# Kernel optimization log

Measured on AMD Instinct MI355X. Metric: run time of the kernel, lower is better.

The kernel has to match this reference:

```python
import jax, jax.numpy as jnp
import numpy as np

THETA = 10000.0
NUM_HEADS = 16


def _rope(x, token_positions):
    # x: [B, H, S, d_k], token_positions: [B, S]
    d_k = x.shape[-1]
    half = d_k // 2
    k = jnp.arange(half, dtype=jnp.float32)
    inv_k = THETA ** (-2.0 * k / d_k)                      # [half]
    pos = token_positions.astype(jnp.float32)              # [B, S]
    angles = pos[..., None] * inv_k                         # [B, S, half]
    angles = jnp.repeat(angles, 2, axis=-1)                 # [B, S, d_k] interleaved
    cos = jnp.cos(angles)[:, None]                          # [B, 1, S, d_k]
    sin = jnp.sin(angles)[:, None]
    x_even = x[..., ::2]
    x_odd = x[..., 1::2]
    r_x = jnp.stack((-x_odd, x_even), axis=-1).reshape(x.shape)
    return x * cos + r_x * sin


def setup_inputs() -> dict:
    key = jax.random.key(0)
    ks = jax.random.split(key, 6)
    B, S, D = 4, 2048, 1024
    delta = 2.0 / np.sqrt(D + D)
    x = jax.random.normal(ks[0], (B, S, D), dtype=jnp.float32)
    Wq = jax.random.normal(ks[1], (D, D), dtype=jnp.float32) * delta
    Wk = jax.random.normal(ks[2], (D, D), dtype=jnp.float32) * delta
    Wv = jax.random.normal(ks[3], (D, D), dtype=jnp.float32) * delta
    Wo = jax.random.normal(ks[4], (D, D), dtype=jnp.float32) * delta
    token_positions = jnp.broadcast_to(jnp.arange(S, dtype=jnp.int64), (B, S))
    return {"x": x, "Wq": Wq, "Wk": Wk, "Wv": Wv, "Wo": Wo,
            "token_positions": token_positions}


def reference(x, Wq, Wk, Wv, Wo, token_positions):
    B, S, D = x.shape
    H = NUM_HEADS
    d_k = D // H

    def split_heads(t):
        return t.reshape(B, S, H, d_k).transpose(0, 2, 1, 3)  # [B, H, S, d_k]

    q = split_heads(x @ Wq.T)
    k = split_heads(x @ Wk.T)
    v = split_heads(x @ Wv.T)

    q = _rope(q, token_positions)
    k = _rope(k, token_positions)

    scores = jnp.einsum('bhqd,bhkd->bhqk', q, k) / jnp.sqrt(jnp.float32(d_k))
    causal = jnp.tril(jnp.ones((S, S), dtype=bool))
    scores = jnp.where(causal, scores, -jnp.inf)
    prob = jax.nn.softmax(scores, axis=-1)
    out = jnp.einsum('bhqk,bhkd->bhqd', prob, v)            # [B, H, S, d_k]
    out = out.transpose(0, 2, 1, 3).reshape(B, S, D)
    return out @ Wo.T
```

## Files before the change

### kernel.cpp

```cpp
#include <hip/hip_runtime.h>
#include <math.h>


typedef __attribute__((ext_vector_type(4))) float f32x4;
typedef __attribute__((ext_vector_type(8))) short bf16x8;

#define MFMA16(A,B,C) __builtin_amdgcn_mfma_f32_16x16x32_bf16((A),(B),(C),0,0,0)

__device__ __forceinline__ unsigned short f2b(float f) {
  unsigned int i = __float_as_uint(f);
  unsigned int r = (i + 0x7fffu + ((i >> 16) & 1u)) >> 16;
  return (unsigned short)r;
}
__device__ __forceinline__ float b2f(unsigned short u) {
  return __uint_as_float(((unsigned int)u) << 16);
}
__device__ __forceinline__ unsigned int cvt_pk_bf16(float lo, float hi) {
  unsigned int r;
  asm("v_cvt_pk_bf16_f32 %0, %1, %2" : "=v"(r) : "v"(lo), "v"(hi));
  return r;
}
__device__ __forceinline__ float exp2_fast(float x) {
  float r;
  asm("v_exp_f32 %0, %1" : "=v"(r) : "v"(x));
  return r;
}

__device__ __forceinline__ void gload_lds16(const void* g, void* l) {
  __builtin_amdgcn_global_load_lds((const __attribute__((address_space(1))) void*)g,
                                   (__attribute__((address_space(3))) void*)l,
                                   16, 0, 0);
}

__global__ __launch_bounds__(256) void cvt_kernel(const float* __restrict__ in,
                                                  unsigned short* __restrict__ out,
                                                  int n8) {
  int i = blockIdx.x * 256 + threadIdx.x;
  if (i >= n8) return;
  const float4* p = reinterpret_cast<const float4*>(in) + (size_t)i * 2;
  float4 a = p[0], b = p[1];
  union { unsigned short us[8]; uint4 v; } u;
  u.us[0] = f2b(a.x); u.us[1] = f2b(a.y); u.us[2] = f2b(a.z); u.us[3] = f2b(a.w);
  u.us[4] = f2b(b.x); u.us[5] = f2b(b.y); u.us[6] = f2b(b.z); u.us[7] = f2b(b.w);
  reinterpret_cast<uint4*>(out)[i] = u.v;
}

__global__ __launch_bounds__(256) void cvt_w_kernel(const float* __restrict__ Wq,
                                                    const float* __restrict__ Wk,
                                                    const float* __restrict__ Wv,
                                                    const float* __restrict__ Wo,
                                                    unsigned short* __restrict__ Wcat,
                                                    unsigned short* __restrict__ Wob) {
  int i = blockIdx.x * 256 + threadIdx.x;
  int mat = i >> 17;
  int off = i & 131071;
  const float* src = (mat == 0) ? Wq : (mat == 1) ? Wk : (mat == 2) ? Wv : Wo;
  unsigned short* dst = (mat < 3) ? (Wcat + ((size_t)mat << 20)) : Wob;
  const float4* p = reinterpret_cast<const float4*>(src) + (size_t)off * 2;
  float4 a = p[0], b = p[1];
  union { unsigned short us[8]; uint4 v; } u;
  u.us[0] = f2b(a.x); u.us[1] = f2b(a.y); u.us[2] = f2b(a.z); u.us[3] = f2b(a.w);
  u.us[4] = f2b(b.x); u.us[5] = f2b(b.y); u.us[6] = f2b(b.z); u.us[7] = f2b(b.w);
  reinterpret_cast<uint4*>(dst)[off] = u.v;
}

template <int EPI, int NTX>
__global__ __launch_bounds__(256) void gemm_bt64(const unsigned short* __restrict__ A,
                                                 const unsigned short* __restrict__ Bw,
                                                 unsigned short* __restrict__ Dq,
                                                 unsigned short* __restrict__ Dk,
                                                 unsigned short* __restrict__ Dv) {
  __shared__ __attribute__((aligned(16))) short a_lds[128 * 64];
  __shared__ __attribute__((aligned(16))) short b_lds[128 * 64];
  const int tid  = threadIdx.x;
  const int lane = tid & 63;
  const int wid  = tid >> 6;
  const int lr = lane & 15, lc = lane >> 4;
  const int wr = wid >> 1, wc = wid & 1;

  const int NB = NTX * 64;
  const int id = blockIdx.x;
  const int nid = (id & 7) * (NB / 8) + (id >> 3);
  const int bx = nid % NTX;
  const int by = nid / NTX;
  const int m0 = by * 128;
  const int n0 = bx * 128;

  f32x4 acc[4][4];
#pragma unroll
  for (int i = 0; i < 4; i++)
#pragma unroll
    for (int j = 0; j < 4; j++) acc[i][j] = (f32x4){0.f, 0.f, 0.f, 0.f};

  const int srow = tid >> 3;
  const int sgx  = (tid & 7) ^ (srow & 7);
  const unsigned short* ag = A  + (size_t)(m0 + srow) * 1024 + sgx * 8;
  const unsigned short* bg = Bw + (size_t)(n0 + srow) * 1024 + sgx * 8;
  short* al = &a_lds[tid * 8];
  short* bl = &b_lds[tid * 8];

  for (int k0 = 0; k0 < 1024; k0 += 64) {
#pragma unroll
    for (int p = 0; p < 4; p++) {
      gload_lds16(ag + k0 + p * 32768, al + p * 2048);
      gload_lds16(bg + k0 + p * 32768, bl + p * 2048);
    }
    __syncthreads();
#pragma unroll
    for (int kc = 0; kc < 2; kc++) {
      bf16x8 af[4], bfr[4];
#pragma unroll
      for (int t = 0; t < 4; t++) {
        const int ra = wr * 64 + t * 16 + lr;
        const int rb = wc * 64 + t * 16 + lr;
        af[t]  = *(const bf16x8*)&a_lds[ra * 64 + (((kc * 4 + lc) ^ (ra & 7)) * 8)];
        bfr[t] = *(const bf16x8*)&b_lds[rb * 64 + (((kc * 4 + lc) ^ (rb & 7)) * 8)];
      }
#pragma unroll
      for (int i = 0; i < 4; i++)
#pragma unroll
        for (int j = 0; j < 4; j++) acc[i][j] = MFMA16(af[i], bfr[j], acc[i][j]);
    }
    __syncthreads();
  }

#pragma unroll
  for (int i = 0; i < 4; i++)
#pragma unroll
    for (int j = 0; j < 4; j++)
#pragma unroll
      for (int r = 0; r < 4; r++) {
        int m = m0 + wr * 64 + i * 16 + lc * 4 + r;
        int n = n0 + wc * 64 + j * 16 + lr;
        float v = acc[i][j][r];
        if (EPI == 1) {
          if (n < 1024) {
            Dq[(size_t)m * 1024 + n] = f2b(v);
          } else if (n < 2048) {
            Dk[(size_t)m * 1024 + (n - 1024)] = f2b(v);
          } else {
            int nl = n - 2048;
            int b = m >> 11, s = m & 2047;
            int h = nl >> 6, d = nl & 63;
            Dv[((size_t)((b * 16 + h) * 64 + d) << 11) + s] = f2b(v);
          }
        } else {
          ((float*)Dq)[(size_t)m * 1024 + n] = v;
        }
      }
}

__global__ __launch_bounds__(256) void rope_kernel(unsigned short* __restrict__ Q,
                                                   unsigned short* __restrict__ K) {
  int idx = blockIdx.x * 256 + threadIdx.x;
  int row = idx >> 7;
  int col = (idx & 127) << 3;
  float pos = (float)(row & 2047);
  int i0 = (col & 63) >> 1;
  float cs[4], sn[4];
#pragma unroll
  for (int p = 0; p < 4; p++) {
    float ang = pos * exp2f(-0.41524101f * (float)(i0 + p));
    sincosf(ang, &sn[p], &cs[p]);
  }
  size_t off = (size_t)row * 1024 + col;
#pragma unroll
  for (int arr = 0; arr < 2; arr++) {
    unsigned short* P = arr ? K : Q;
    const float sc = arr ? 1.0f : 0.18033688011112042f;
    union { unsigned short us[8]; uint4 v; } u;
    u.v = *(const uint4*)(P + off);
#pragma unroll
    for (int p = 0; p < 4; p++) {
      float e = b2f(u.us[2 * p]), o = b2f(u.us[2 * p + 1]);
      u.us[2 * p]     = f2b((e * cs[p] - o * sn[p]) * sc);
      u.us[2 * p + 1] = f2b((o * cs[p] + e * sn[p]) * sc);
    }
    *(uint4*)(P + off) = u.v;
  }
}

__global__ __launch_bounds__(512, 4) void attn_kernel(const unsigned short* __restrict__ Q,
                                                      const unsigned short* __restrict__ K,
                                                      const unsigned short* __restrict__ Vt,
                                                      unsigned short* __restrict__ O) {
  __shared__ __attribute__((aligned(16))) char K_lds[2][8192];
  __shared__ __attribute__((aligned(16))) char V_lds[2][8192];
  __shared__ __attribute__((aligned(16))) short P_lds[8][16][72];

  const int t    = threadIdx.x;
  const int lane = t & 63;
  const int wid  = t >> 6;
  const int lr = lane & 15, lc = (lane >> 4) & 3;
  const int lc4 = lc * 4;
  const int sbase = lane & 48;
  const int rswz = (lr & 7) << 4;
  const int csw0 = (lc * 16) ^ rswz;
  const int csw1 = (64 + lc * 16) ^ rswz;

  const int id  = blockIdx.y * 8 + blockIdx.x;
  const int nid = (id & 7) * 64 + (id >> 3);
  const int bx  = nid & 7;
  const int bh  = nid >> 3;
  const int b   = bh >> 4;

  const unsigned short* Qb = Q  + (size_t)b * 2048 * 1024 + (bh & 15) * 64;
  const unsigned short* Kb = K  + (size_t)b * 2048 * 1024 + (bh & 15) * 64;
  const unsigned short* Vb = Vt + (size_t)bh * 64 * 2048;

  const int srow = t >> 3;
  const int scol = ((t & 7) * 16) ^ ((srow & 7) << 4);
  const char* kstage = (const char*)Kb + (size_t)srow * 2048 + scol;
  const char* vstage = (const char*)Vb + (size_t)srow * 4096 + scol;
  const int t16 = t * 16;

  short* myP = &P_lds[wid][0][0];

  gload_lds16(kstage, &K_lds[0][t16]);
  gload_lds16(vstage, &V_lds[0][t16]);
  __syncthreads();
  int buf = 0;

  for (int half = 0; half < 2; half++) {
    const int band = half ? (15 - bx) : bx;
    const int n = 2 * band + 2;
    const int qw = band * 128 + wid * 16;

    bf16x8 qf[2];
#pragma unroll
    for (int c = 0; c < 2; c++)
      qf[c] = *(const bf16x8*)(Qb + (size_t)(qw + lr) * 1024 + c * 32 + lc * 8);

    f32x4 acc[4];
#pragma unroll
    for (int d = 0; d < 4; d++) acc[d] = (f32x4){0.f, 0.f, 0.f, 0.f};
    float mrow = -1e30f, lrow = 0.f;

    for (int tt = 0; tt < n; tt++) {
      const int kv0 = tt << 6;

      if (tt + 1 < n) {
        const size_t ko = (size_t)(kv0 + 64);
        gload_lds16(kstage + ko * 2048, &K_lds[buf ^ 1][t16]);
        gload_lds16(vstage + ko * 2,    &V_lds[buf ^ 1][t16]);
      } else if (half == 0) {
        gload_lds16(kstage, &K_lds[buf ^ 1][t16]);
        gload_lds16(vstage, &V_lds[buf ^ 1][t16]);
      }

      const char* kb = K_lds[buf] + lr * 128;
      const char* vb = V_lds[buf] + lr * 128;

      f32x4 st[4];
#pragma unroll
      for (int nt = 0; nt < 4; nt++) {
        bf16x8 ka0 = *(const bf16x8*)(kb + nt * 2048 + csw0);
        bf16x8 ka1 = *(const bf16x8*)(kb + nt * 2048 + csw1);
        f32x4 s4 = (f32x4){0.f, 0.f, 0.f, 0.f};
        s4 = MFMA16(ka0, qf[0], s4);
        s4 = MFMA16(ka1, qf[1], s4);
        st[nt] = s4;
      }

      if (kv0 + 64 > qw) {
        const int lim = qw + lr - kv0 - lc4;
#pragma unroll
        for (int nt = 0; nt < 4; nt++)
#pragma unroll
          for (int r = 0; r < 4; r++)
            if (nt * 16 + r > lim) st[nt][r] = -1e30f;
      }

      float t0 = fmaxf(fmaxf(st[0][0], st[0][1]), fmaxf(st[0][2], st[0][3]));
      float t1 = fmaxf(fmaxf(st[1][0], st[1][1]), fmaxf(st[1][2], st[1][3]));
      float t2 = fmaxf(fmaxf(st[2][0], st[2][1]), fmaxf(st[2][2], st[2][3]));
      float t3 = fmaxf(fmaxf(st[3][0], st[3][1]), fmaxf(st[3][2], st[3][3]));
      float tm = fmaxf(fmaxf(t0, t1), fmaxf(t2, t3));
      tm = fmaxf(tm, __shfl_xor(tm, 16));
      tm = fmaxf(tm, __shfl_xor(tm, 32));
      float mnew = fmaxf(mrow, tm);
      float scale = exp2_fast(mrow - mnew);
      mrow = mnew;

#pragma unroll
      for (int nt = 0; nt < 4; nt++) {
#pragma unroll
        for (int r = 0; r < 4; r++) st[nt][r] = exp2_fast(st[nt][r] - mrow);
        uint2 w;
        w.x = cvt_pk_bf16(st[nt][0], st[nt][1]);
        w.y = cvt_pk_bf16(st[nt][2], st[nt][3]);
        *(uint2*)&myP[lr * 72 + nt * 16 + lc4] = w;
      }

      float s0 = (st[0][0] + st[0][1]) + (st[0][2] + st[0][3]);
      float s1 = (st[1][0] + st[1][1]) + (st[1][2] + st[1][3]);
      float s2 = (st[2][0] + st[2][1]) + (st[2][2] + st[2][3]);
      float s3 = (st[3][0] + st[3][1]) + (st[3][2] + st[3][3]);
      float psum = (s0 + s1) + (s2 + s3);
      psum += __shfl_xor(psum, 16);
      psum += __shfl_xor(psum, 32);
      lrow = lrow * scale + psum;

      float sc4[4];
#pragma unroll
      for (int r = 0; r < 4; r++) sc4[r] = __shfl(scale, sbase | (lc4 + r));
#pragma unroll
      for (int d = 0; d < 4; d++) {
        acc[d][0] *= sc4[0]; acc[d][1] *= sc4[1];
        acc[d][2] *= sc4[2]; acc[d][3] *= sc4[3];
      }

#pragma unroll
      for (int c = 0; c < 2; c++) {
        bf16x8 pa = *(const bf16x8*)&myP[lr * 72 + c * 32 + lc * 8];
        const int csw = c ? csw1 : csw0;
#pragma unroll
        for (int d = 0; d < 4; d++) {
          bf16x8 vf = *(const bf16x8*)(vb + d * 2048 + csw);
          acc[d] = MFMA16(pa, vf, acc[d]);
        }
      }

      __syncthreads();
      buf ^= 1;
    }

    float linv[4];
#pragma unroll
    for (int r = 0; r < 4; r++)
      linv[r] = __builtin_amdgcn_rcpf(__shfl(lrow, sbase | (lc4 + r)));

    const int hcol = (bh & 15) * 64;
#pragma unroll
    for (int d = 0; d < 4; d++)
#pragma unroll
      for (int r = 0; r < 4; r++) {
        int q = qw + lc4 + r;
        O[(size_t)(b * 2048 + q) * 1024 + hcol + d * 16 + lr] = f2b(acc[d][r] * linv[r]);
      }
  }
}

extern "C" void kernel_launch(void* const* d_in, const int* in_sizes, int n_in,
                              void* d_out, int out_size, void* d_ws, size_t ws_size,
                              hipStream_t stream) {
  const float* x  = (const float*)d_in[0];
  const float* Wq = (const float*)d_in[1];
  const float* Wk = (const float*)d_in[2];
  const float* Wv = (const float*)d_in[3];
  const float* Wo = (const float*)d_in[4];
  float* out = (float*)d_out;

  char* ws = (char*)d_ws;
  const size_t MB = 1u << 20;
  unsigned short* xb   = (unsigned short*)(ws);
  unsigned short* Wcat = (unsigned short*)(ws + 16 * MB);
  unsigned short* Wob  = (unsigned short*)(ws + 22 * MB);
  unsigned short* Qb   = (unsigned short*)(ws + 24 * MB);
  unsigned short* Kb   = (unsigned short*)(ws + 40 * MB);
  unsigned short* Vtb  = (unsigned short*)(ws + 56 * MB);
  unsigned short* Ob   = xb;

  cvt_kernel<<<4096, 256, 0, stream>>>(x, xb, 1048576);
  cvt_w_kernel<<<2048, 256, 0, stream>>>(Wq, Wk, Wv, Wo, Wcat, Wob);

  gemm_bt64<1, 24><<<1536, 256, 0, stream>>>(xb, Wcat, Qb, Kb, Vtb);

  rope_kernel<<<4096, 256, 0, stream>>>(Qb, Kb);

  attn_kernel<<<dim3(8, 64), 512, 0, stream>>>(Qb, Kb, Vtb, Ob);

  gemm_bt64<2, 8><<<512, 256, 0, stream>>>(Ob, Wob, (unsigned short*)out, nullptr, nullptr);
}
```

Before: 198.9 us.

## Fuse RoPE into QKV GEMM epilogue and double-buffer GEMM LDS tiles

Removes the separate RoPE kernel by applying the rotation and Q scaling in the QKV GEMM epilogue. Adjacent even/odd columns are exchanged with a lane shuffle, and sin/cos are computed per element. Also double-buffers the A/B LDS tiles so the next K-slice global-to-LDS load is issued before the current slice's MFMAs, dropping one barrier per iteration. LDS use doubles to 64KB per block, which may reduce occupancy. The epilogue now does many sincosf calls, which may be costly.

```diff
diff --git a/kernel.cpp b/kernel.cpp
--- a/kernel.cpp
+++ b/kernel.cpp
@@ -70,8 +70,8 @@
                                                  unsigned short* __restrict__ Dq,
                                                  unsigned short* __restrict__ Dk,
                                                  unsigned short* __restrict__ Dv) {
-  __shared__ __attribute__((aligned(16))) short a_lds[128 * 64];
-  __shared__ __attribute__((aligned(16))) short b_lds[128 * 64];
+  __shared__ __attribute__((aligned(16))) short a_lds[2][128 * 64];
+  __shared__ __attribute__((aligned(16))) short b_lds[2][128 * 64];
   const int tid  = threadIdx.x;
   const int lane = tid & 63;
   const int wid  = tid >> 6;
@@ -96,16 +96,24 @@
   const int sgx  = (tid & 7) ^ (srow & 7);
   const unsigned short* ag = A  + (size_t)(m0 + srow) * 1024 + sgx * 8;
   const unsigned short* bg = Bw + (size_t)(n0 + srow) * 1024 + sgx * 8;
-  short* al = &a_lds[tid * 8];
-  short* bl = &b_lds[tid * 8];
-
+
+#pragma unroll
+  for (int p = 0; p < 4; p++) {
+    gload_lds16(ag + p * 32768, &a_lds[0][tid * 8 + p * 2048]);
+    gload_lds16(bg + p * 32768, &b_lds[0][tid * 8 + p * 2048]);
+  }
+  __syncthreads();
+
+  int buf = 0;
   for (int k0 = 0; k0 < 1024; k0 += 64) {
-#pragma unroll
-    for (int p = 0; p < 4; p++) {
-      gload_lds16(ag + k0 + p * 32768, al + p * 2048);
-      gload_lds16(bg + k0 + p * 32768, bl + p * 2048);
+    if (k0 + 64 < 1024) {
+      const int nb = buf ^ 1;
+#pragma unroll
+      for (int p = 0; p < 4; p++) {
+        gload_lds16(ag + (k0 + 64) + p * 32768, &a_lds[nb][tid * 8 + p * 2048]);
+        gload_lds16(bg + (k0 + 64) + p * 32768, &b_lds[nb][tid * 8 + p * 2048]);
+      }
     }
-    __syncthreads();
 #pragma unroll
     for (int kc = 0; kc < 2; kc++) {
       bf16x8 af[4], bfr[4];
@@ -113,8 +121,8 @@
       for (int t = 0; t < 4; t++) {
         const int ra = wr * 64 + t * 16 + lr;
         const int rb = wc * 64 + t * 16 + lr;
-        af[t]  = *(const bf16x8*)&a_lds[ra * 64 + (((kc * 4 + lc) ^ (ra & 7)) * 8)];
-        bfr[t] = *(const bf16x8*)&b_lds[rb * 64 + (((kc * 4 + lc) ^ (rb & 7)) * 8)];
+        af[t]  = *(const bf16x8*)&a_lds[buf][ra * 64 + (((kc * 4 + lc) ^ (ra & 7)) * 8)];
+        bfr[t] = *(const bf16x8*)&b_lds[buf][rb * 64 + (((kc * 4 + lc) ^ (rb & 7)) * 8)];
       }
 #pragma unroll
       for (int i = 0; i < 4; i++)
@@ -122,61 +130,57 @@
         for (int j = 0; j < 4; j++) acc[i][j] = MFMA16(af[i], bfr[j], acc[i][j]);
     }
     __syncthreads();
+    buf ^= 1;
   }
 
-#pragma unroll
-  for (int i = 0; i < 4; i++)
-#pragma unroll
-    for (int j = 0; j < 4; j++)
-#pragma unroll
-      for (int r = 0; r < 4; r++) {
-        int m = m0 + wr * 64 + i * 16 + lc * 4 + r;
-        int n = n0 + wc * 64 + j * 16 + lr;
-        float v = acc[i][j][r];
-        if (EPI == 1) {
-          if (n < 1024) {
-            Dq[(size_t)m * 1024 + n] = f2b(v);
-          } else if (n < 2048) {
-            Dk[(size_t)m * 1024 + (n - 1024)] = f2b(v);
-          } else {
-            int nl = n - 2048;
-            int b = m >> 11, s = m & 2047;
-            int h = nl >> 6, d = nl & 63;
-            Dv[((size_t)((b * 16 + h) * 64 + d) << 11) + s] = f2b(v);
-          }
-        } else {
-          ((float*)Dq)[(size_t)m * 1024 + n] = v;
+  if (EPI == 2) {
+    float* D = (float*)Dq;
+#pragma unroll
+    for (int i = 0; i < 4; i++)
+#pragma unroll
+      for (int j = 0; j < 4; j++)
+#pragma unroll
+        for (int r = 0; r < 4; r++) {
+          int m = m0 + wr * 64 + i * 16 + lc * 4 + r;
+          int n = n0 + wc * 64 + j * 16 + lr;
+          D[(size_t)m * 1024 + n] = acc[i][j][r];
         }
-      }
-}
-
-__global__ __launch_bounds__(256) void rope_kernel(unsigned short* __restrict__ Q,
-                                                   unsigned short* __restrict__ K) {
-  int idx = blockIdx.x * 256 + threadIdx.x;
-  int row = idx >> 7;
-  int col = (idx & 127) << 3;
-  float pos = (float)(row & 2047);
-  int i0 = (col & 63) >> 1;
-  float cs[4], sn[4];
-#pragma unroll
-  for (int p = 0; p < 4; p++) {
-    float ang = pos * exp2f(-0.41524101f * (float)(i0 + p));
-    sincosf(ang, &sn[p], &cs[p]);
-  }
-  size_t off = (size_t)row * 1024 + col;
-#pragma unroll
-  for (int arr = 0; arr < 2; arr++) {
-    unsigned short* P = arr ? K : Q;
-    const float sc = arr ? 1.0f : 0.18033688011112042f;
-    union { unsigned short us[8]; uint4 v; } u;
-    u.v = *(const uint4*)(P + off);
-#pragma unroll
-    for (int p = 0; p < 4; p++) {
-      float e = b2f(u.us[2 * p]), o = b2f(u.us[2 * p + 1]);
-      u.us[2 * p]     = f2b((e * cs[p] - o * sn[p]) * sc);
-      u.us[2 * p + 1] = f2b((o * cs[p] + e * sn[p]) * sc);
+  } else if (n0 >= 2048) {
+#pragma unroll
+    for (int i = 0; i < 4; i++)
+#pragma unroll
+      for (int j = 0; j < 4; j++)
+#pragma unroll
+        for (int r = 0; r < 4; r++) {
+          int m = m0 + wr * 64 + i * 16 + lc * 4 + r;
+          int nl = (n0 - 2048) + wc * 64 + j * 16 + lr;
+          int b = m >> 11, s = m & 2047;
+          int h = nl >> 6, d = nl & 63;
+          Dv[((size_t)((b * 16 + h) * 64 + d) << 11) + s] = f2b(acc[i][j][r]);
+        }
+  } else {
+    const bool isQ = (n0 < 1024);
+    const float qs = isQ ? 0.18033688011112042f : 1.0f;
+    unsigned short* D = isQ ? Dq : Dk;
+    const int odd = lane & 1;
+#pragma unroll
+    for (int j = 0; j < 4; j++) {
+      const int i0 = (j * 16 + lr) >> 1;
+      const float inv = exp2f(-0.41524101f * (float)i0);
+#pragma unroll
+      for (int i = 0; i < 4; i++)
+#pragma unroll
+        for (int r = 0; r < 4; r++) {
+          int m = m0 + wr * 64 + i * 16 + lc * 4 + r;
+          int n = n0 + wc * 64 + j * 16 + lr;
+          float cs, sn;
+          sincosf((float)(m & 2047) * inv, &sn, &cs);
+          float v = acc[i][j][r];
+          float pv = __shfl_xor(v, 1);
+          float res = (v * cs + (odd ? pv : -pv) * sn) * qs;
+          D[(size_t)m * 1024 + (n & 1023)] = f2b(res);
+        }
     }
-    *(uint4*)(P + off) = u.v;
   }
 }
 
@@ -366,8 +370,6 @@
 
   gemm_bt64<1, 24><<<1536, 256, 0, stream>>>(xb, Wcat, Qb, Kb, Vtb);
 
-  rope_kernel<<<4096, 256, 0, stream>>>(Qb, Kb);
-
   attn_kernel<<<dim3(8, 64), 512, 0, stream>>>(Qb, Kb, Vtb, Ob);
 
   gemm_bt64<2, 8><<<512, 256, 0, stream>>>(Ob, Wob, (unsigned short*)out, nullptr, nullptr);
```

Measured after the change: 672.0 us. 238% more time.
